# Kernel tuning notes

Hardware: AMD Instinct MI355X
Metric: run time of the kernel (lower is better)

The kernel has to match this reference:

```python
import jax, jax.numpy as jnp
import numpy as np

VOCAB, EMB = 30000, 300
HEADS, DPH = 8, 50
AD = HEADS * DPH            # att_dim_total = 400
MAX_LINES, MAX_WPL = 128, 32
BATCH = 16
NEG = 1e7                   # padding-mask penalty, matches torch source


def _split_heads(x):
    # [N, S, AD] -> [N, H, S, D]
    return x.reshape(x.shape[0], -1, HEADS, DPH).transpose(0, 2, 1, 3)


def _attention(q, k, v, mask_q=None, mask_k=None, mask_v=None):
    # Faithful port of MTHiSAN._attention. Note the (oddly named) torch masks:
    #   mask_q masks the KEY axis of scores, mask_k/mask_v zero the QUERY axis.
    scale = float(np.sqrt(q.shape[-1]))
    scores = jnp.einsum('bhqd,bhkd->bhqk', q, k) / scale
    if mask_q is not None:
        scores = scores - NEG * (~mask_q)[:, None, None, :].astype(scores.dtype)
    w = jax.nn.softmax(scores, axis=-1)
    if mask_k is not None:
        w = w * mask_k[:, None, :, None].astype(w.dtype)
    out = jnp.einsum('bhqk,bhkd->bhqd', w, v)
    if mask_v is not None:
        out = out * mask_v[:, None, :, None].astype(out.dtype)
    return out


def _forward(docs, emb, wq_w, wq_b, wk_w, wk_b, wv_w, wv_b, w_tgt,
             lq_w, lq_b, lk_w, lk_b, lv_w, lv_b, l_tgt,
             fc1_w, fc1_b, fc2_w, fc2_b):
    B = docs.shape[0]
    d = docs[:, :MAX_LINES * MAX_WPL].reshape(B * MAX_LINES, MAX_WPL)
    mask_w = d != 0                               # [B*L, W]
    mask_l = mask_w.sum(-1) != 0                  # [B*L]  non-empty lines
    # NOTE: instead of gathering non-empty lines (data-dependent shape), we keep
    # full shapes; masked word attention yields exact zeros for empty lines,
    # equivalent to the torch scatter into new_zeros.
    we = emb[d]                                   # [B*L, W, E] (dropout = eval/no-op)
    wq = jax.nn.elu(_split_heads(we @ wq_w + wq_b))
    wk = jax.nn.elu(_split_heads(we @ wk_w + wk_b))
    wv = jax.nn.elu(_split_heads(we @ wv_w + wv_b))
    watt = _attention(wq, wk, wv, mask_w, mask_w, mask_w)   # [B*L,H,W,D]
    # learned word-level target query (Linear(1, AD)(ones) == weight vector)
    tgt = jnp.broadcast_to(w_tgt.reshape(1, HEADS, 1, DPH),
                           (B * MAX_LINES, HEADS, 1, DPH))
    line_e = _attention(tgt, wk, watt, mask_q=mask_w)       # [B*L,H,1,D]
    line_e = line_e.transpose(0, 2, 1, 3).reshape(B * MAX_LINES, AD)
    line_e = line_e * mask_l[:, None].astype(line_e.dtype)  # zero empty lines
    line_e = line_e.reshape(B, MAX_LINES, AD)
    mask_l2 = mask_l.reshape(B, MAX_LINES)
    lq = jax.nn.elu(_split_heads(line_e @ lq_w + lq_b))
    lk = jax.nn.elu(_split_heads(line_e @ lk_w + lk_b))
    lv = jax.nn.elu(_split_heads(line_e @ lv_w + lv_b))
    latt = _attention(lq, lk, lv, mask_l2, mask_l2, mask_l2)  # [B,H,L,D]
    dtgt = jnp.broadcast_to(l_tgt.reshape(1, HEADS, 1, DPH), (B, HEADS, 1, DPH))
    doc_e = _attention(dtgt, lk, latt, mask_q=mask_l2)        # [B,H,1,D]
    doc_e = doc_e.transpose(0, 2, 1, 3).reshape(B, AD)
    logits1 = doc_e @ fc1_w + fc1_b   # task 'site'      [B,70]
    logits2 = doc_e @ fc2_w + fc2_b   # task 'histology' [B,512]
    return jnp.concatenate([logits1, logits2], axis=1)


def setup_inputs() -> dict:
    key = jax.random.key(0)
    ks = jax.random.split(key, 20)
    xavier = lambda k, i, o: (jax.random.normal(k, (i, o), jnp.float32)
                              * np.float32(np.sqrt(2.0 / (i + o))))
    emb = jax.random.normal(ks[0], (VOCAB, EMB), jnp.float32) * 0.02
    emb = emb.at[0].set(0.0)  # padding row zeroed as in __init__
    docs = jax.random.randint(ks[1], (BATCH, MAX_LINES * MAX_WPL), 0, VOCAB)
    z = lambda n: jnp.zeros((n,), jnp.float32)
    return dict(
        docs=docs, emb=emb,
        wq_w=xavier(ks[2], EMB, AD), wq_b=z(AD),
        wk_w=xavier(ks[3], EMB, AD), wk_b=z(AD),
        wv_w=xavier(ks[4], EMB, AD), wv_b=z(AD),
        w_tgt=jax.random.uniform(ks[5], (AD,), jnp.float32),
        lq_w=xavier(ks[6], AD, AD), lq_b=z(AD),
        lk_w=xavier(ks[7], AD, AD), lk_b=z(AD),
        lv_w=xavier(ks[8], AD, AD), lv_b=z(AD),
        l_tgt=jax.random.uniform(ks[9], (AD,), jnp.float32),
        fc1_w=xavier(ks[10], AD, 70), fc1_b=z(70),
        fc2_w=xavier(ks[11], AD, 512), fc2_b=z(512),
    )


def reference(docs, emb, wq_w, wq_b, wk_w, wk_b, wv_w, wv_b, w_tgt,
              lq_w, lq_b, lk_w, lk_b, lv_w, lv_b, l_tgt,
              fc1_w, fc1_b, fc2_w, fc2_b):
    return _forward(docs, emb, wq_w, wq_b, wk_w, wk_b, wv_w, wv_b, w_tgt,
                    lq_w, lq_b, lk_w, lk_b, lv_w, lv_b, l_tgt,
                    fc1_w, fc1_b, fc2_w, fc2_b)
```

## Files before the change

kernel.cpp:

```cpp
#include <hip/hip_runtime.h>
#include <math.h>

#define NLINES 2048
#define WPL 32
#define EMBD 300
#define AD 400
#define NH 8
#define DPH 50
#define QKV_S 52
#define SC_S 36
#define BATCH 16
#define LPD 128
#define NCOLS 1200
#define NPAD 1280
#define HBLK 4992
#define QP 54

typedef __bf16 bf16;
typedef bf16  v8bf  __attribute__((ext_vector_type(8)));
typedef float v16f  __attribute__((ext_vector_type(16)));

__device__ __forceinline__ float elu(float x) {
    return x > 0.f ? x : expm1f(x);
}
__device__ __forceinline__ float elu_fast(float x) {
    return x > 0.f ? x : (__expf(x) - 1.f);
}

__device__ __forceinline__ v8bf ntload8(const bf16* p) {
    return __builtin_nontemporal_load((const v8bf*)p);
}

#define SCALE 7.0710678118654755f

__global__ void split_rows_packed(const float* __restrict__ src,
                                  bf16* __restrict__ pk,
                                  int rows, int K, int K2)
{
    long idx = (long)blockIdx.x * 256 + threadIdx.x;
    if (idx >= (long)rows * K2) return;
    int r = (int)(idx / K2), k = (int)(idx - (long)r * K2);
    float x = (k < K) ? src[(long)r * K + k] : 0.f;
    bf16 h = (bf16)x;
    float hf = (float)h;
    bf16 l = (bf16)(x - hf);
    const long p = ((long)r * (K2 >> 3) + (k >> 3)) * 16 + (k & 7);
    pk[p] = h; pk[p + 8] = l;
}

__global__ void split_wt_packed(const float* __restrict__ W0, const float* __restrict__ W1,
                                const float* __restrict__ W2,
                                const float* __restrict__ B0, const float* __restrict__ B1,
                                const float* __restrict__ B2,
                                bf16* __restrict__ pk,
                                float* __restrict__ biasCat, int K, int K2)
{
    long idx = (long)blockIdx.x * 256 + threadIdx.x;
    if (idx >= (long)NPAD * K2) return;
    int n = (int)(idx / K2), k = (int)(idx - (long)n * K2);
    float x = 0.f;
    if (k < K && n < NCOLS) {
        int p = n / 400, c = n - p * 400;
        const float* W = (p == 0) ? W0 : (p == 1) ? W1 : W2;
        x = W[(long)k * 400 + c];
    }
    bf16 h = (bf16)x;
    float hf = (float)h;
    bf16 l = (bf16)(x - hf);
    const long pidx = ((long)(k >> 3) * NPAD + n) * 16 + (k & 7);
    pk[pidx] = h; pk[pidx + 8] = l;
    if (k == 0) {
        float b = 0.f;
        if (n < NCOLS) {
            int p = n / 400, c = n - p * 400;
            const float* Bp = (p == 0) ? B0 : (p == 1) ? B1 : B2;
            b = Bp[c];
        }
        biasCat[n] = b;
    }
}

__launch_bounds__(512, 2)
__global__ void fused_word(const bf16* __restrict__ Ap,
                           const int* __restrict__ docs,
                           const bf16* __restrict__ Bp,
                           const float* __restrict__ biasCat,
                           const float* __restrict__ w_tgt,
                           float* __restrict__ line_e, float* __restrict__ mask_l)
{
    __shared__ __align__(16) bf16 Alds[40 * 2 * 32 * 8];
    __shared__ __align__(16) float qkv[3][32][QP];
    __shared__ float sc[32 * 33];
    __shared__ float part[16][33];
    __shared__ float vpart[8][64];
    __shared__ float tw[WPL];
    __shared__ float coefA[WPL];
    __shared__ float cw[WPL];
    __shared__ float tg[52];
    __shared__ float msk[WPL];
    __shared__ float mls_s;

    const int tid = threadIdx.x;
    const int line = blockIdx.x;

    if (tid < WPL) msk[tid] = (docs[line * WPL + tid] != 0) ? 1.f : 0.f;
    __syncthreads();
    if (tid == 0) {
        float m = 0.f;
        for (int w = 0; w < WPL; ++w) m = fmaxf(m, msk[w]);
        mls_s = m;
        mask_l[line] = m;
    }

    for (int slot = tid; slot < 40 * 2 * 32; slot += 512) {
        const int row = slot & 31;
        const int hl  = (slot >> 5) & 1;
        const int kf  = slot >> 6;
        const int token = docs[line * WPL + row];
        *(v8bf*)&Alds[slot * 8] = ntload8(&Ap[((long)token * 40 + kf) * 16 + hl * 8]);
    }
    __syncthreads();

    const int wv = tid >> 6;
    const int lane = tid & 63;
    const int half = lane >> 5, r32 = lane & 31;

    for (int h = 0; h < NH; ++h) {
        if (wv < 6) {
            const int proj = wv >> 1;
            const int c0 = proj * 400 + h * 50 + (wv & 1) * 32;
            v16f a0 = (v16f)0.f, a1 = (v16f)0.f, a2 = (v16f)0.f;
            #pragma unroll 4
            for (int s = 0; s < 20; ++s) {
                const int kf = 2 * s + half;
                const v8bf fah = *(const v8bf*)&Alds[((kf * 2 + 0) * 32 + r32) * 8];
                const v8bf fal = *(const v8bf*)&Alds[((kf * 2 + 1) * 32 + r32) * 8];
                const bf16* bg = Bp + ((long)kf * NPAD + c0 + r32) * 16;
                const v8bf fbh = *(const v8bf*)&bg[0];
                const v8bf fbl = *(const v8bf*)&bg[8];
                a0 = __builtin_amdgcn_mfma_f32_32x32x16_bf16(fah, fbh, a0, 0, 0, 0);
                a1 = __builtin_amdgcn_mfma_f32_32x32x16_bf16(fah, fbl, a1, 0, 0, 0);
                a2 = __builtin_amdgcn_mfma_f32_32x32x16_bf16(fal, fbh, a2, 0, 0, 0);
            }
            const int d = (wv & 1) * 32 + r32;
            if (d < DPH) {
                const float bv = biasCat[c0 + r32];
                #pragma unroll
                for (int rg = 0; rg < 16; ++rg) {
                    const int row = (rg & 3) + 8 * (rg >> 2) + 4 * half;
                    qkv[proj][row][d] = elu_fast(a0[rg] + a1[rg] + a2[rg] + bv);
                }
            }
        } else {
            const int t = tid - 384;
            if (t < 96) {
                const int p = t / 32, row = t & 31;
                qkv[p][row][50] = 0.f; qkv[p][row][51] = 0.f;
                qkv[p][row][52] = 0.f; qkv[p][row][53] = 0.f;
            } else if (t >= 96 && t < 148) {
                const int i = t - 96;
                tg[i] = (i < DPH) ? w_tgt[h * DPH + i] : 0.f;
            }
        }
        __syncthreads();

        const float* q   = &qkv[0][0][0];
        const float* kk_ = &qkv[1][0][0];
        const float* vv_ = &qkv[2][0][0];

        const int j = tid >> 4, kg = tid & 15;
        float2 qv[27];
        #pragma unroll
        for (int i = 0; i < 27; ++i) qv[i] = *(const float2*)&q[j * QP + 2 * i];

        float e2[2];
        float m = -1e30f;
        #pragma unroll
        for (int c = 0; c < 2; ++c) {
            const int kk = kg * 2 + c;
            const float* kr = &kk_[kk * QP];
            float s = 0.f;
            #pragma unroll
            for (int i = 0; i < 27; ++i)
                s += qv[i].x * kr[2 * i] + qv[i].y * kr[2 * i + 1];
            s = s / SCALE - 1e7f * (1.f - msk[kk]);
            e2[c] = s;
            m = fmaxf(m, s);
        }
        m = fmaxf(m, __shfl_xor(m, 1, 16));
        m = fmaxf(m, __shfl_xor(m, 2, 16));
        m = fmaxf(m, __shfl_xor(m, 4, 16));
        m = fmaxf(m, __shfl_xor(m, 8, 16));
        float rsum = 0.f;
        #pragma unroll
        for (int c = 0; c < 2; ++c) { e2[c] = __expf(e2[c] - m); rsum += e2[c]; }
        rsum += __shfl_xor(rsum, 1, 16);
        rsum += __shfl_xor(rsum, 2, 16);
        rsum += __shfl_xor(rsum, 4, 16);
        rsum += __shfl_xor(rsum, 8, 16);
        sc[j * 33 + kg * 2]     = e2[0];
        sc[j * 33 + kg * 2 + 1] = e2[1];

        if (tid < WPL) {
            const float* kr = &kk_[tid * QP];
            float s = 0.f;
            #pragma unroll
            for (int i = 0; i < 25; ++i)
                s += tg[2 * i] * kr[2 * i] + tg[2 * i + 1] * kr[2 * i + 1];
            s = s / SCALE - 1e7f * (1.f - msk[tid]);
            float tm = s;
            #pragma unroll
            for (int off = 16; off >= 1; off >>= 1) tm = fmaxf(tm, __shfl_xor(tm, off, 32));
            const float te = __expf(s - tm);
            float tsum = te;
            #pragma unroll
            for (int off = 16; off >= 1; off >>= 1) tsum += __shfl_xor(tsum, off, 32);
            tw[tid] = te / tsum;
        }
        __syncthreads();

        if (kg == 0) coefA[j] = tw[j] * msk[j] / rsum;
        __syncthreads();

        {
            const int k = tid & 31, jg = tid >> 5;
            const int j0 = jg * 2;
            part[jg][k] = coefA[j0] * sc[j0 * 33 + k]
                        + coefA[j0 + 1] * sc[(j0 + 1) * 33 + k];
        }
        __syncthreads();
        if (tid < WPL) {
            float cv = 0.f;
            #pragma unroll
            for (int g = 0; g < 16; ++g) cv += part[g][tid];
            cw[tid] = cv;
        }
        __syncthreads();

        {
            const int d = tid & 63, kh = tid >> 6;
            float acc = 0.f;
            if (d < QP) {
                #pragma unroll
                for (int t = 0; t < 4; ++t) {
                    const int k = kh * 4 + t;
                    acc += cw[k] * vv_[k * QP + d];
                }
            }
            vpart[kh][d] = acc;
        }
        __syncthreads();
        if (tid < DPH) {
            float o = 0.f;
            #pragma unroll
            for (int g = 0; g < 8; ++g) o += vpart[g][tid];
            line_e[(long)line * AD + h * DPH + tid] = o * mls_s;
        }
        __syncthreads();
    }
}

__launch_bounds__(256, 4)
__global__ void mfma_gemm(const bf16* __restrict__ Ap,
                          const int* __restrict__ docs,
                          const bf16* __restrict__ Bp,
                          const float* __restrict__ biasCat,
                          float* __restrict__ C, int K2, int word_layout)
{
    __shared__ int tok[128];

    const int tid = threadIdx.x;

    const int total = (int)(gridDim.x * gridDim.y);
    int flat = (int)(blockIdx.y * gridDim.x + blockIdx.x);
    if ((total & 7) == 0) flat = (flat & 7) * (total >> 3) + (flat >> 3);
    const int bx = flat % (int)gridDim.x;
    const int by = flat / (int)gridDim.x;
    const int row0 = by * 128;
    const int n0 = bx * 128;

    if (tid < 128) tok[tid] = docs ? docs[row0 + tid] : (row0 + tid);
    __syncthreads();

    const int wv = tid >> 6, lane = tid & 63;
    const int half = lane >> 5, r32 = lane & 31;
    const int wm0 = (wv >> 1) * 64, wn0 = (wv & 1) * 64;

    const int colA = n0 + wn0 + r32;
    const int colB = colA + 32;

    const long a0 = (long)tok[wm0 + r32]      * ((long)K2 * 2);
    const long a1 = (long)tok[wm0 + 32 + r32] * ((long)K2 * 2);

    v16f acc[2][2];
    #pragma unroll
    for (int a = 0; a < 2; ++a)
        #pragma unroll
        for (int b = 0; b < 2; ++b) acc[a][b] = (v16f)0.f;

    const int nk = K2 >> 5;
    for (int kt = 0; kt < nk; ++kt) {
        #pragma unroll
        for (int ks = 0; ks < 2; ++ks) {
            const int k0 = kt * 32 + (ks * 2 + half) * 8;
            const bf16* bg = Bp + (long)(k0 >> 3) * NPAD * 16;
            const long ka = (long)k0 * 2;
            v8bf fb_h[2], fb_l[2], fa_h[2], fa_l[2];
            fb_h[0] = *(const v8bf*)&bg[(long)colA * 16];
            fb_l[0] = *(const v8bf*)&bg[(long)colA * 16 + 8];
            fb_h[1] = *(const v8bf*)&bg[(long)colB * 16];
            fb_l[1] = *(const v8bf*)&bg[(long)colB * 16 + 8];
            fa_h[0] = *(const v8bf*)&Ap[a0 + ka];
            fa_l[0] = *(const v8bf*)&Ap[a0 + ka + 8];
            fa_h[1] = *(const v8bf*)&Ap[a1 + ka];
            fa_l[1] = *(const v8bf*)&Ap[a1 + ka + 8];

            #pragma unroll
            for (int mt = 0; mt < 2; ++mt)
                #pragma unroll
                for (int nt = 0; nt < 2; ++nt)
                    acc[mt][nt] = __builtin_amdgcn_mfma_f32_32x32x16_bf16(fa_h[mt], fb_h[nt], acc[mt][nt], 0, 0, 0);
            #pragma unroll
            for (int mt = 0; mt < 2; ++mt)
                #pragma unroll
                for (int nt = 0; nt < 2; ++nt)
                    acc[mt][nt] = __builtin_amdgcn_mfma_f32_32x32x16_bf16(fa_h[mt], fb_l[nt], acc[mt][nt], 0, 0, 0);
            #pragma unroll
            for (int mt = 0; mt < 2; ++mt)
                #pragma unroll
                for (int nt = 0; nt < 2; ++nt)
                    acc[mt][nt] = __builtin_amdgcn_mfma_f32_32x32x16_bf16(fa_l[mt], fb_h[nt], acc[mt][nt], 0, 0, 0);
        }
    }

    if (word_layout) {
        #pragma unroll
        for (int nt = 0; nt < 2; ++nt) {
            const int col = n0 + wn0 + nt * 32 + r32;
            if (col >= NCOLS) continue;
            const float bv = biasCat[col];
            const int p = col / 400;
            const int rem = col - p * 400;
            const int hh = rem / 50;
            const int d  = rem - hh * 50;
            #pragma unroll
            for (int mt = 0; mt < 2; ++mt) {
                const int rbase = row0 + wm0 + mt * 32 + 4 * half;
                #pragma unroll
                for (int rg = 0; rg < 16; ++rg) {
                    const int row = rbase + (rg & 3) + 8 * (rg >> 2);
                    const int ln = row >> 5, r = row & 31;
                    const long base = (((long)ln * NH + hh) * 3 + p) * 1664 + r * 52;
                    const float x = acc[mt][nt][rg] + bv;
                    C[base + d] = elu_fast(x);
                    if (d == 49) {
                        float2 z; z.x = 0.f; z.y = 0.f;
                        *(float2*)&C[base + 50] = z;
                    }
                }
            }
        }
    } else {
        #pragma unroll
        for (int nt = 0; nt < 2; ++nt) {
            const int col = n0 + wn0 + nt * 32 + r32;
            if (col >= NCOLS) continue;
            const float bv = biasCat[col];
            #pragma unroll
            for (int mt = 0; mt < 2; ++mt) {
                const int rbase = row0 + wm0 + mt * 32 + 4 * half;
                #pragma unroll
                for (int rg = 0; rg < 16; ++rg) {
                    const int row = rbase + (rg & 3) + 8 * (rg >> 2);
                    const float x = acc[mt][nt][rg] + bv;
                    C[(long)row * NCOLS + col] = elu_fast(x);
                }
            }
        }
    }
}

__launch_bounds__(256)
__global__ void line_attn2(const float* __restrict__ Q, const float* __restrict__ Kp,
                           const float* __restrict__ Vp,
                           long DS, long HS, long LS,
                           const float* __restrict__ l_tgt, const float* __restrict__ mask_l,
                           float* __restrict__ doc_e)
{
    __shared__ float kl[LPD * 52];
    __shared__ float sc[64 * 130];
    __shared__ float ml[LPD];
    __shared__ float tw[LPD];
    __shared__ float cw[LPD];
    __shared__ float coefA[64];
    __shared__ float pm[4 * 64];
    __shared__ float ps[4 * 64];
    __shared__ float tg[52];
    __shared__ float rr[2];
    __shared__ float vpart[2][64];

    const int tid = threadIdx.x;
    const int doc = blockIdx.x >> 3;
    const int h = blockIdx.x & 7;
    const float* qbase = Q + doc * DS + h * HS;
    const float* kbase = Kp + doc * DS + h * HS;
    const float* vbase = Vp + doc * DS + h * HS;

    if (tid < LPD) { ml[tid] = mask_l[doc * LPD + tid]; cw[tid] = 0.f; }
    if (tid < 52) tg[tid] = (tid < DPH) ? l_tgt[h * DPH + tid] : 0.f;
    for (int idx = tid; idx < LPD * 52; idx += 256) {
        const int r = idx / 52, d = idx - r * 52;
        kl[idx] = (d < DPH) ? kbase[(long)r * LS + d] : 0.f;
    }
    __syncthreads();

    if (tid < LPD) {
        const float* kr = &kl[tid * 52];
        float s = 0.f;
        #pragma unroll
        for (int i = 0; i < 25; ++i)
            s += tg[2 * i] * kr[2 * i] + tg[2 * i + 1] * kr[2 * i + 1];
        tw[tid] = s / SCALE - 1e7f * (1.f - ml[tid]);
    }
    __syncthreads();
    if (tid < 64) {
        float a = fmaxf(tw[tid], tw[64 + tid]);
        #pragma unroll
        for (int off = 32; off >= 1; off >>= 1) a = fmaxf(a, __shfl_xor(a, off));
        if (tid == 0) rr[0] = a;
    }
    __syncthreads();
    if (tid < 64) {
        const float tm2 = rr[0];
        float a = __expf(tw[tid] - tm2) + __expf(tw[64 + tid] - tm2);
        #pragma unroll
        for (int off = 32; off >= 1; off >>= 1) a += __shfl_xor(a, off);
        if (tid == 0) rr[1] = a;
    }
    __syncthreads();
    if (tid < LPD) tw[tid] = __expf(tw[tid] - rr[0]) / rr[1];
    __syncthreads();

    const int j2 = tid & 63;
    const int kq = tid >> 6;

    for (int g = 0; g < 2; ++g) {
        const int j = g * 64 + j2;
        float2 qv[25];
        #pragma unroll
        for (int i = 0; i < 25; ++i)
            qv[i] = *(const float2*)(qbase + (long)j * LS + 2 * i);

        float m = -1e30f;
        for (int c = 0; c < 32; ++c) {
            const int k = kq * 32 + c;
            const float* kr = &kl[k * 52];
            float s = 0.f;
            #pragma unroll
            for (int i = 0; i < 25; ++i)
                s += qv[i].x * kr[2 * i] + qv[i].y * kr[2 * i + 1];
            s = s / SCALE - 1e7f * (1.f - ml[k]);
            sc[j2 * 130 + k] = s;
            m = fmaxf(m, s);
        }
        pm[kq * 64 + j2] = m;
        __syncthreads();
        const float rowm = fmaxf(fmaxf(pm[j2], pm[64 + j2]),
                                 fmaxf(pm[128 + j2], pm[192 + j2]));
        float sum = 0.f;
        for (int c = 0; c < 32; ++c) {
            const int k = kq * 32 + c;
            const float e = __expf(sc[j2 * 130 + k] - rowm);
            sc[j2 * 130 + k] = e;
            sum += e;
        }
        ps[kq * 64 + j2] = sum;
        __syncthreads();
        if (kq == 0) {
            const float rs = ps[j2] + ps[64 + j2] + ps[128 + j2] + ps[192 + j2];
            coefA[j2] = tw[j] * ml[j] / rs;
        }
        __syncthreads();
        if (tid < LPD) {
            float cv = 0.f;
            for (int jj = 0; jj < 64; ++jj)
                cv += coefA[jj] * sc[jj * 130 + tid];
            cw[tid] += cv;
        }
        __syncthreads();
    }

    const int d = tid & 63;
    const int half = (tid >> 6) & 1;
    if (tid < 128 && d < DPH) {
        float acc = 0.f;
        for (int k = half * 64; k < half * 64 + 64; ++k)
            acc += cw[k] * vbase[(long)k * LS + d];
        vpart[half][d] = acc;
    }
    __syncthreads();
    if (tid < DPH)
        doc_e[doc * AD + h * DPH + tid] = vpart[0][tid] + vpart[1][tid];
}

__launch_bounds__(256)
__global__ void word_attn(const float* __restrict__ qkv, const int* __restrict__ docs,
                          const float* __restrict__ w_tgt,
                          float* __restrict__ line_e, float* __restrict__ mask_l)
{
    __shared__ float qs[WPL * QKV_S];
    __shared__ float ks[WPL * QKV_S];
    __shared__ float vs[WPL * QKV_S];
    __shared__ float sc[WPL * SC_S];
    __shared__ float ts[WPL], tw[WPL], cw[WPL], msk[WPL];
    __shared__ float mls;

    const int tid = threadIdx.x;
    const int line = blockIdx.x;

    if (tid < WPL) msk[tid] = (docs[line * WPL + tid] != 0) ? 1.f : 0.f;
    __syncthreads();
    if (tid == 0) {
        float ml = 0.f;
        for (int w = 0; w < WPL; ++w) ml = fmaxf(ml, msk[w]);
        mls = ml;
        mask_l[line] = ml;
    }
    for (int h = 0; h < NH; ++h) {
        for (int idx = tid; idx < WPL * DPH; idx += 256) {
            const int r = idx / DPH, d = idx - r * DPH;
            const size_t base = (size_t)(line * WPL + r) * NCOLS + h * DPH + d;
            qs[r * QKV_S + d] = qkv[base];
            ks[r * QKV_S + d] = qkv[base + 400];
            vs[r * QKV_S + d] = qkv[base + 800];
        }
        __syncthreads();
        {
            const int j = tid >> 3, kg = tid & 7;
            #pragma unroll
            for (int c = 0; c < 4; ++c) {
                const int kk = kg * 4 + c;
                float s = 0.f;
                for (int dd = 0; dd < DPH; ++dd)
                    s += qs[j * QKV_S + dd] * ks[kk * QKV_S + dd];
                sc[j * SC_S + kk] = s / SCALE - 1e7f * (1.f - msk[kk]);
            }
        }
        if (tid < WPL) {
            float s = 0.f;
            for (int dd = 0; dd < DPH; ++dd)
                s += w_tgt[h * DPH + dd] * ks[tid * QKV_S + dd];
            ts[tid] = s / SCALE - 1e7f * (1.f - msk[tid]);
        }
        __syncthreads();
        if (tid < WPL) {
            const int j = tid;
            float m = -1e30f;
            for (int kk = 0; kk < WPL; ++kk) m = fmaxf(m, sc[j * SC_S + kk]);
            float sum = 0.f;
            for (int kk = 0; kk < WPL; ++kk) {
                const float e = expf(sc[j * SC_S + kk] - m);
                sc[j * SC_S + kk] = e;
                sum += e;
            }
            const float inv = 1.f / sum;
            for (int kk = 0; kk < WPL; ++kk) sc[j * SC_S + kk] *= inv;
        } else if (tid == WPL) {
            float m = -1e30f;
            for (int jj = 0; jj < WPL; ++jj) m = fmaxf(m, ts[jj]);
            float sum = 0.f;
            for (int jj = 0; jj < WPL; ++jj) { const float e = expf(ts[jj] - m); tw[jj] = e; sum += e; }
            const float inv = 1.f / sum;
            for (int jj = 0; jj < WPL; ++jj) tw[jj] *= inv;
        }
        __syncthreads();
        if (tid < WPL) {
            const int kk = tid;
            float c = 0.f;
            for (int jj = 0; jj < WPL; ++jj) c += tw[jj] * msk[jj] * sc[jj * SC_S + kk];
            cw[kk] = c;
        }
        __syncthreads();
        if (tid < DPH) {
            float acc = 0.f;
            for (int kk = 0; kk < WPL; ++kk) acc += cw[kk] * vs[kk * QKV_S + tid];
            line_e[line * AD + h * DPH + tid] = acc * mls;
        }
        __syncthreads();
    }
}

__launch_bounds__(256, 2)
__global__ void gemm_qkv(const float* __restrict__ Asrc,
                         const int* __restrict__ docs,
                         const float* __restrict__ emb,
                         const float* __restrict__ W0, const float* __restrict__ W1,
                         const float* __restrict__ W2,
                         const float* __restrict__ B0, const float* __restrict__ B1,
                         const float* __restrict__ B2,
                         float* __restrict__ C, int M, int K)
{
    __shared__ __align__(16) float As[32][132];
    __shared__ __align__(16) float Bs[32][132];

    const int tid = threadIdx.x;
    const int row0 = blockIdx.x * 128;
    const int n0 = blockIdx.y * 128;
    const int tc = tid & 15, tr = tid >> 4;

    float acc[2][2][4][4];
    #pragma unroll
    for (int a = 0; a < 2; ++a)
        #pragma unroll
        for (int b = 0; b < 2; ++b)
            #pragma unroll
            for (int c = 0; c < 4; ++c)
                #pragma unroll
                for (int d = 0; d < 4; ++d) acc[a][b][c][d] = 0.f;

    const int ma = tid & 127;
    const int kq = tid >> 7;
    const float* arow;
    if (docs) arow = emb + (size_t)docs[row0 + ma] * EMBD;
    else      arow = Asrc + (size_t)(row0 + ma) * K;

    const int gcol = n0 + ma;
    const int p = gcol / 400;
    const int ccol = gcol - p * 400;
    const float* Wp = (p == 0) ? W0 : (p == 1) ? W1 : W2;
    const bool colv = gcol < NCOLS;

    const int nk = (K + 31) >> 5;
    for (int ck = 0; ck < nk; ++ck) {
        const int k0 = ck * 32;
        #pragma unroll
        for (int f = 0; f < 4; ++f) {
            const int kl = kq * 16 + f * 4;
            const int kg = k0 + kl;
            float4 v = make_float4(0.f, 0.f, 0.f, 0.f);
            if (kg < K) v = *(const float4*)(arow + kg);
            As[kl + 0][ma] = v.x;
            As[kl + 1][ma] = v.y;
            As[kl + 2][ma] = v.z;
            As[kl + 3][ma] = v.w;
        }
        #pragma unroll
        for (int i = 0; i < 16; ++i) {
            const int kl = kq * 16 + i;
            const int kg = k0 + kl;
            float v = 0.f;
            if (colv && kg < K) v = Wp[(size_t)kg * 400 + ccol];
            Bs[kl][ma] = v;
        }
        __syncthreads();

        #pragma unroll 8
        for (int k = 0; k < 32; ++k) {
            const float4 a0 = *(const float4*)&As[k][tr * 4];
            const float4 a1 = *(const float4*)&As[k][64 + tr * 4];
            const float4 b0 = *(const float4*)&Bs[k][tc * 4];
            const float4 b1 = *(const float4*)&Bs[k][64 + tc * 4];
            const float ar[2][4] = {{a0.x, a0.y, a0.z, a0.w}, {a1.x, a1.y, a1.z, a1.w}};
            const float br[2][4] = {{b0.x, b0.y, b0.z, b0.w}, {b1.x, b1.y, b1.z, b1.w}};
            #pragma unroll
            for (int im = 0; im < 2; ++im)
                #pragma unroll
                for (int in_ = 0; in_ < 2; ++in_)
                    #pragma unroll
                    for (int rr = 0; rr < 4; ++rr)
                        #pragma unroll
                        for (int cc = 0; cc < 4; ++cc)
                            acc[im][in_][rr][cc] += ar[im][rr] * br[in_][cc];
        }
        __syncthreads();
    }

    #pragma unroll
    for (int in_ = 0; in_ < 2; ++in_) {
        const int ncol = n0 + in_ * 64 + tc * 4;
        if (ncol >= NCOLS) continue;
        const int pj = ncol / 400;
        const int cj = ncol - pj * 400;
        const float* Bp = (pj == 0) ? B0 : (pj == 1) ? B1 : B2;
        const float4 bv = *(const float4*)(Bp + cj);
        #pragma unroll
        for (int im = 0; im < 2; ++im) {
            #pragma unroll
            for (int rr = 0; rr < 4; ++rr) {
                const int row = row0 + im * 64 + tr * 4 + rr;
                float4 o;
                o.x = elu(acc[im][in_][rr][0] + bv.x);
                o.y = elu(acc[im][in_][rr][1] + bv.y);
                o.z = elu(acc[im][in_][rr][2] + bv.z);
                o.w = elu(acc[im][in_][rr][3] + bv.w);
                *(float4*)(C + (size_t)row * NCOLS + ncol) = o;
            }
        }
    }
}

__global__ void logits_kernel(const float* __restrict__ doc_e,
                              const float* __restrict__ fc1_w, const float* __restrict__ fc1_b,
                              const float* __restrict__ fc2_w, const float* __restrict__ fc2_b,
                              float* __restrict__ out)
{
    int o = blockIdx.x * blockDim.x + threadIdx.x;
    if (o >= BATCH * 582) return;
    int b = o / 582, jj = o - b * 582;
    const float* de = doc_e + b * AD;
    float acc;
    if (jj < 70) {
        acc = fc1_b[jj];
        for (int k = 0; k < AD; ++k) acc += de[k] * fc1_w[k * 70 + jj];
    } else {
        int j2 = jj - 70;
        acc = fc2_b[j2];
        for (int k = 0; k < AD; ++k) acc += de[k] * fc2_w[k * 512 + j2];
    }
    out[o] = acc;
}

extern "C" void kernel_launch(void* const* d_in, const int* in_sizes, int n_in,
                              void* d_out, int out_size, void* d_ws, size_t ws_size,
                              hipStream_t stream) {
    const int*   docs  = (const int*)  d_in[0];
    const float* emb   = (const float*)d_in[1];
    const float* wq_w  = (const float*)d_in[2];
    const float* wq_b  = (const float*)d_in[3];
    const float* wk_w  = (const float*)d_in[4];
    const float* wk_b  = (const float*)d_in[5];
    const float* wv_w  = (const float*)d_in[6];
    const float* wv_b  = (const float*)d_in[7];
    const float* w_tgt = (const float*)d_in[8];
    const float* lq_w  = (const float*)d_in[9];
    const float* lq_b  = (const float*)d_in[10];
    const float* lk_w  = (const float*)d_in[11];
    const float* lk_b  = (const float*)d_in[12];
    const float* lv_w  = (const float*)d_in[13];
    const float* lv_b  = (const float*)d_in[14];
    const float* l_tgt = (const float*)d_in[15];
    const float* fc1_w = (const float*)d_in[16];
    const float* fc1_b = (const float*)d_in[17];
    const float* fc2_w = (const float*)d_in[18];
    const float* fc2_b = (const float*)d_in[19];
    float* out = (float*)d_out;
    float* ws = (float*)d_ws;

    const long O_LINE_E = 0;
    const long O_MASK_L = 819200;
    const long O_DOC_E  = 821248;
    const long O_BIAS_W = 827648;
    const long O_BIAS_L = 828928;
    const long O_EMB_H  = 830208;
    const long O_WTW_H  = 10430208;
    const long O_WTL_H  = 10839808;
    const long O_LE_H   = 11372288;
    const long O_R      = 12224256;

    const long LINE_QKV_FL = (long)NLINES * NCOLS;
    long ws_fl = (long)(ws_size / 4);
    long Rcap = ws_fl - O_R;

    if (Rcap >= LINE_QKV_FL) {
        float* line_e = ws + O_LINE_E;
        float* mask_l = ws + O_MASK_L;
        float* doc_e  = ws + O_DOC_E;
        float* bias_w = ws + O_BIAS_W;
        float* bias_l = ws + O_BIAS_L;
        bf16* embp = (bf16*)(ws + O_EMB_H);
        bf16* wtwp = (bf16*)(ws + O_WTW_H);
        bf16* wtlp = (bf16*)(ws + O_WTL_H);
        bf16* lep  = (bf16*)(ws + O_LE_H);
        float* R   = ws + O_R;

        split_rows_packed<<<(30000L * 320 + 255) / 256, 256, 0, stream>>>(emb, embp, 30000, 300, 320);
        split_wt_packed<<<((long)NPAD * 320 + 255) / 256, 256, 0, stream>>>(wq_w, wk_w, wv_w,
                                                                            wq_b, wk_b, wv_b,
                                                                            wtwp, bias_w, 300, 320);
        split_wt_packed<<<((long)NPAD * 416 + 255) / 256, 256, 0, stream>>>(lq_w, lk_w, lv_w,
                                                                            lq_b, lk_b, lv_b,
                                                                            wtlp, bias_l, 400, 416);

        fused_word<<<NLINES, 512, 0, stream>>>(embp, docs, wtwp, bias_w, w_tgt,
                                               line_e, mask_l);

        split_rows_packed<<<((long)NLINES * 416 + 255) / 256, 256, 0, stream>>>(line_e, lep,
                                                                                NLINES, 400, 416);
        dim3 g2(10, NLINES / 128);
        mfma_gemm<<<g2, 256, 0, stream>>>(lep, nullptr, wtlp, bias_l, R, 416, 0);
        line_attn2<<<BATCH * NH, 256, 0, stream>>>(R, R + 400, R + 800,
                                                   (long)LPD * NCOLS, (long)DPH, (long)NCOLS,
                                                   l_tgt, mask_l, doc_e);
        logits_kernel<<<(BATCH * 582 + 255) / 256, 256, 0, stream>>>(doc_e, fc1_w, fc1_b,
                                                                     fc2_w, fc2_b, out);
    } else {
        const long F_FIXED = 827648;
        const long PER_LINE_FL = (long)WPL * NCOLS;
        float* line_e = ws;
        float* mask_l = ws + 819200;
        float* doc_e  = ws + 821248;
        float* R      = ws + F_FIXED;
        long Rcap2 = ws_fl - F_FIXED;

        long maxl = Rcap2 / PER_LINE_FL;
        if (maxl > NLINES) maxl = NLINES;
        long maxl4 = (maxl / 4) * 4;
        int nc = (int)((NLINES + maxl4 - 1) / maxl4);
        int chunk = (int)((NLINES + nc - 1) / nc);
        chunk = ((chunk + 3) / 4) * 4;

        for (int c0 = 0; c0 < NLINES; c0 += chunk) {
            int cl = NLINES - c0 < chunk ? NLINES - c0 : chunk;
            dim3 g1((cl * 32) / 128, 10);
            gemm_qkv<<<g1, 256, 0, stream>>>(nullptr, docs + (size_t)c0 * WPL, emb,
                                             wq_w, wk_w, wv_w, wq_b, wk_b, wv_b,
                                             R, cl * 32, EMBD);
            word_attn<<<cl, 256, 0, stream>>>(R, docs + (size_t)c0 * WPL, w_tgt,
                                              line_e + (size_t)c0 * AD, mask_l + c0);
        }
        dim3 g2(16, 10);
        gemm_qkv<<<g2, 256, 0, stream>>>(line_e, nullptr, emb,
                                         lq_w, lk_w, lv_w, lq_b, lk_b, lv_b,
                                         R, NLINES, AD);
        line_attn2<<<BATCH * NH, 256, 0, stream>>>(R, R + 400, R + 800,
                                                   (long)LPD * NCOLS, (long)DPH, (long)NCOLS,
                                                   l_tgt, mask_l, doc_e);
        logits_kernel<<<(BATCH * 582 + 255) / 256, 256, 0, stream>>>(doc_e, fc1_w, fc1_b,
                                                                     fc2_w, fc2_b, out);
    }
}
```

Before: 574.6 us.

## Restructure word attention epilogue to cut barriers using 32-lane shuffle reductions

Rewrites the per-head attention tail of fused_word so each 32-lane group computes scores for two query rows plus the target row against its key, then does the softmax reductions with shuffles instead of going through shared memory. The final weighted sum over V is also done with shuffle reductions. Together these remove several shared arrays and about four __syncthreads per head. The cost is more redundant key loads and extra shuffle traffic per thread, since each thread now computes three dot products.

New measurement: 604.7 us. +5.2%, slower.

```diff
diff --git a/kernel.cpp b/kernel.cpp
--- a/kernel.cpp
+++ b/kernel.cpp
@@ -90,13 +90,8 @@
 {
     __shared__ __align__(16) bf16 Alds[40 * 2 * 32 * 8];
     __shared__ __align__(16) float qkv[3][32][QP];
-    __shared__ float sc[32 * 33];
     __shared__ float part[16][33];
-    __shared__ float vpart[8][64];
-    __shared__ float tw[WPL];
-    __shared__ float coefA[WPL];
-    __shared__ float cw[WPL];
-    __shared__ float tg[52];
+    __shared__ float tg[56];
     __shared__ float msk[WPL];
     __shared__ float mls_s;
 
@@ -157,104 +152,76 @@
                 const int p = t / 32, row = t & 31;
                 qkv[p][row][50] = 0.f; qkv[p][row][51] = 0.f;
                 qkv[p][row][52] = 0.f; qkv[p][row][53] = 0.f;
-            } else if (t >= 96 && t < 148) {
+            } else if (t >= 96 && t < 152) {
                 const int i = t - 96;
                 tg[i] = (i < DPH) ? w_tgt[h * DPH + i] : 0.f;
             }
         }
         __syncthreads();
 
-        const float* q   = &qkv[0][0][0];
-        const float* kk_ = &qkv[1][0][0];
-        const float* vv_ = &qkv[2][0][0];
-
-        const int j = tid >> 4, kg = tid & 15;
-        float2 qv[27];
-        #pragma unroll
-        for (int i = 0; i < 27; ++i) qv[i] = *(const float2*)&q[j * QP + 2 * i];
-
-        float e2[2];
-        float m = -1e30f;
-        #pragma unroll
-        for (int c = 0; c < 2; ++c) {
-            const int kk = kg * 2 + c;
-            const float* kr = &kk_[kk * QP];
-            float s = 0.f;
-            #pragma unroll
-            for (int i = 0; i < 27; ++i)
-                s += qv[i].x * kr[2 * i] + qv[i].y * kr[2 * i + 1];
-            s = s / SCALE - 1e7f * (1.f - msk[kk]);
-            e2[c] = s;
-            m = fmaxf(m, s);
-        }
-        m = fmaxf(m, __shfl_xor(m, 1, 16));
-        m = fmaxf(m, __shfl_xor(m, 2, 16));
-        m = fmaxf(m, __shfl_xor(m, 4, 16));
-        m = fmaxf(m, __shfl_xor(m, 8, 16));
-        float rsum = 0.f;
-        #pragma unroll
-        for (int c = 0; c < 2; ++c) { e2[c] = __expf(e2[c] - m); rsum += e2[c]; }
-        rsum += __shfl_xor(rsum, 1, 16);
-        rsum += __shfl_xor(rsum, 2, 16);
-        rsum += __shfl_xor(rsum, 4, 16);
-        rsum += __shfl_xor(rsum, 8, 16);
-        sc[j * 33 + kg * 2]     = e2[0];
-        sc[j * 33 + kg * 2 + 1] = e2[1];
-
-        if (tid < WPL) {
-            const float* kr = &kk_[tid * QP];
-            float s = 0.f;
-            #pragma unroll
-            for (int i = 0; i < 25; ++i)
-                s += tg[2 * i] * kr[2 * i] + tg[2 * i + 1] * kr[2 * i + 1];
-            s = s / SCALE - 1e7f * (1.f - msk[tid]);
-            float tm = s;
-            #pragma unroll
-            for (int off = 16; off >= 1; off >>= 1) tm = fmaxf(tm, __shfl_xor(tm, off, 32));
-            const float te = __expf(s - tm);
-            float tsum = te;
-            #pragma unroll
-            for (int off = 16; off >= 1; off >>= 1) tsum += __shfl_xor(tsum, off, 32);
-            tw[tid] = te / tsum;
-        }
-        __syncthreads();
-
-        if (kg == 0) coefA[j] = tw[j] * msk[j] / rsum;
-        __syncthreads();
-
         {
-            const int k = tid & 31, jg = tid >> 5;
-            const int j0 = jg * 2;
-            part[jg][k] = coefA[j0] * sc[j0 * 33 + k]
-                        + coefA[j0 + 1] * sc[(j0 + 1) * 33 + k];
-        }
-        __syncthreads();
-        if (tid < WPL) {
-            float cv = 0.f;
-            #pragma unroll
-            for (int g = 0; g < 16; ++g) cv += part[g][tid];
-            cw[tid] = cv;
+            const int slot = tid >> 5;
+            const int k = tid & 31;
+            const int j0 = slot * 2, j1 = j0 + 1;
+            const float* Krow = &qkv[1][k][0];
+            const float* Q0   = &qkv[0][j0][0];
+            const float* Q1   = &qkv[0][j1][0];
+            float s0 = 0.f, s1 = 0.f, st = 0.f;
+            #pragma unroll
+            for (int i = 0; i < 27; ++i) {
+                const float2 kv = *(const float2*)&Krow[2 * i];
+                const float2 q0 = *(const float2*)&Q0[2 * i];
+                const float2 q1 = *(const float2*)&Q1[2 * i];
+                const float2 tv = *(const float2*)&tg[2 * i];
+                s0 += q0.x * kv.x + q0.y * kv.y;
+                s1 += q1.x * kv.x + q1.y * kv.y;
+                st += tv.x * kv.x + tv.y * kv.y;
+            }
+            const float pen = 1e7f * (1.f - msk[k]);
+            s0 = s0 / SCALE - pen;
+            s1 = s1 / SCALE - pen;
+            st = st / SCALE - pen;
+
+            float m0 = s0, m1 = s1, mt = st;
+            #pragma unroll
+            for (int off = 16; off >= 1; off >>= 1) {
+                m0 = fmaxf(m0, __shfl_xor(m0, off, 32));
+                m1 = fmaxf(m1, __shfl_xor(m1, off, 32));
+                mt = fmaxf(mt, __shfl_xor(mt, off, 32));
+            }
+            const float e0 = __expf(s0 - m0);
+            const float e1 = __expf(s1 - m1);
+            const float et = __expf(st - mt);
+            float r0 = e0, r1 = e1, rt = et;
+            #pragma unroll
+            for (int off = 16; off >= 1; off >>= 1) {
+                r0 += __shfl_xor(r0, off, 32);
+                r1 += __shfl_xor(r1, off, 32);
+                rt += __shfl_xor(rt, off, 32);
+            }
+            const float tw_k = et / rt;
+            const float c0 = __shfl(tw_k, j0, 32) * msk[j0] / r0;
+            const float c1 = __shfl(tw_k, j1, 32) * msk[j1] / r1;
+            part[slot][k] = c0 * e0 + c1 * e1;
         }
         __syncthreads();
 
         {
-            const int d = tid & 63, kh = tid >> 6;
-            float acc = 0.f;
-            if (d < QP) {
-                #pragma unroll
-                for (int t = 0; t < 4; ++t) {
-                    const int k = kh * 4 + t;
-                    acc += cw[k] * vv_[k * QP + d];
-                }
-            }
-            vpart[kh][d] = acc;
-        }
-        __syncthreads();
-        if (tid < DPH) {
-            float o = 0.f;
-            #pragma unroll
-            for (int g = 0; g < 8; ++g) o += vpart[g][tid];
-            line_e[(long)line * AD + h * DPH + tid] = o * mls_s;
+            const int slot = tid >> 5;
+            const int k = tid & 31;
+            float cwk = 0.f;
+            #pragma unroll
+            for (int g = 0; g < 16; ++g) cwk += part[g][k];
+            #pragma unroll
+            for (int di = 0; di < 4; ++di) {
+                const int d = slot * 4 + di;
+                float p = (d < DPH) ? cwk * qkv[2][k][d] : 0.f;
+                #pragma unroll
+                for (int off = 16; off >= 1; off >>= 1)
+                    p += __shfl_xor(p, off, 32);
+                if (k == 0 && d < DPH)
+                    line_e[(long)line * AD + h * DPH + d] = p * mls_s;
+            }
         }
         __syncthreads();
     }
```

## Process two lines per fused_word block to reuse weight fragments across lines

Applied to the files above, without the earlier changes.

Each fused_word block now handles two document lines. Every B-weight fragment loaded from global memory feeds MFMAs for both lines, so weight traffic per line is halved. The attention phase splits the 512 threads into two 256-thread halves, one per line, with each thread covering more keys. The price is double the LDS footprint, more accumulator registers, launch bounds lowered to one block per CU, and half as many blocks, which may reduce occupancy and latency hiding.

Result: slower. 632.0 us (+10.0%).

```diff
diff --git a/kernel.cpp b/kernel.cpp
--- a/kernel.cpp
+++ b/kernel.cpp
@@ -80,7 +80,7 @@
     }
 }
 
-__launch_bounds__(512, 2)
+__launch_bounds__(512, 1)
 __global__ void fused_word(const bf16* __restrict__ Ap,
                            const int* __restrict__ docs,
                            const bf16* __restrict__ Bp,
@@ -88,36 +88,44 @@
                            const float* __restrict__ w_tgt,
                            float* __restrict__ line_e, float* __restrict__ mask_l)
 {
-    __shared__ __align__(16) bf16 Alds[40 * 2 * 32 * 8];
-    __shared__ __align__(16) float qkv[3][32][QP];
-    __shared__ float sc[32 * 33];
-    __shared__ float part[16][33];
-    __shared__ float vpart[8][64];
-    __shared__ float tw[WPL];
-    __shared__ float coefA[WPL];
-    __shared__ float cw[WPL];
-    __shared__ float tg[52];
-    __shared__ float msk[WPL];
-    __shared__ float mls_s;
+    __shared__ __align__(16) bf16 Alds[2][40 * 2 * 32 * 8];
+    __shared__ __align__(16) float qkv[2][3][32][QP];
+    __shared__ float sc[2][32 * 33];
+    __shared__ float part[2][8][33];
+    __shared__ float vpart[2][4][64];
+    __shared__ float tw[2][WPL];
+    __shared__ float coefA[2][WPL];
+    __shared__ float cw[2][WPL];
+    __shared__ float tg[56];
+    __shared__ float msk[2][WPL];
+    __shared__ float mls_s[2];
 
     const int tid = threadIdx.x;
-    const int line = blockIdx.x;
-
-    if (tid < WPL) msk[tid] = (docs[line * WPL + tid] != 0) ? 1.f : 0.f;
-    __syncthreads();
-    if (tid == 0) {
+    const int line0 = blockIdx.x * 2;
+
+    if (tid < 2 * WPL) {
+        const int li = tid >> 5, w = tid & 31;
+        msk[li][w] = (docs[(line0 + li) * WPL + w] != 0) ? 1.f : 0.f;
+    }
+    __syncthreads();
+    if (tid < 2) {
         float m = 0.f;
-        for (int w = 0; w < WPL; ++w) m = fmaxf(m, msk[w]);
-        mls_s = m;
-        mask_l[line] = m;
-    }
-
-    for (int slot = tid; slot < 40 * 2 * 32; slot += 512) {
-        const int row = slot & 31;
-        const int hl  = (slot >> 5) & 1;
-        const int kf  = slot >> 6;
-        const int token = docs[line * WPL + row];
-        *(v8bf*)&Alds[slot * 8] = ntload8(&Ap[((long)token * 40 + kf) * 16 + hl * 8]);
+        for (int w = 0; w < WPL; ++w) m = fmaxf(m, msk[tid][w]);
+        mls_s[tid] = m;
+        mask_l[line0 + tid] = m;
+    }
+
+    for (int g = tid; g < 2 * 2560; g += 512) {
+        const int li = g >> 11;
+        const int slot = g & 2047;
+        const int li2 = g / 2560;
+        const int s2  = g - li2 * 2560;
+        const int row = s2 & 31;
+        const int hl  = (s2 >> 5) & 1;
+        const int kf  = s2 >> 6;
+        const int token = docs[(line0 + li2) * WPL + row];
+        (void)li; (void)slot;
+        *(v8bf*)&Alds[li2][s2 * 8] = ntload8(&Ap[((long)token * 40 + kf) * 16 + hl * 8]);
     }
     __syncthreads();
 
@@ -129,18 +137,26 @@
         if (wv < 6) {
             const int proj = wv >> 1;
             const int c0 = proj * 400 + h * 50 + (wv & 1) * 32;
-            v16f a0 = (v16f)0.f, a1 = (v16f)0.f, a2 = (v16f)0.f;
+            v16f p0 = (v16f)0.f, p1 = (v16f)0.f, p2 = (v16f)0.f;
+            v16f q0 = (v16f)0.f, q1 = (v16f)0.f, q2 = (v16f)0.f;
             #pragma unroll 4
             for (int s = 0; s < 20; ++s) {
                 const int kf = 2 * s + half;
-                const v8bf fah = *(const v8bf*)&Alds[((kf * 2 + 0) * 32 + r32) * 8];
-                const v8bf fal = *(const v8bf*)&Alds[((kf * 2 + 1) * 32 + r32) * 8];
                 const bf16* bg = Bp + ((long)kf * NPAD + c0 + r32) * 16;
                 const v8bf fbh = *(const v8bf*)&bg[0];
                 const v8bf fbl = *(const v8bf*)&bg[8];
-                a0 = __builtin_amdgcn_mfma_f32_32x32x16_bf16(fah, fbh, a0, 0, 0, 0);
-                a1 = __builtin_amdgcn_mfma_f32_32x32x16_bf16(fah, fbl, a1, 0, 0, 0);
-                a2 = __builtin_amdgcn_mfma_f32_32x32x16_bf16(fal, fbh, a2, 0, 0, 0);
+                const int ea = ((kf * 2 + 0) * 32 + r32) * 8;
+                const int eb = ((kf * 2 + 1) * 32 + r32) * 8;
+                const v8bf fah0 = *(const v8bf*)&Alds[0][ea];
+                const v8bf fal0 = *(const v8bf*)&Alds[0][eb];
+                const v8bf fah1 = *(const v8bf*)&Alds[1][ea];
+                const v8bf fal1 = *(const v8bf*)&Alds[1][eb];
+                p0 = __builtin_amdgcn_mfma_f32_32x32x16_bf16(fah0, fbh, p0, 0, 0, 0);
+                q0 = __builtin_amdgcn_mfma_f32_32x32x16_bf16(fah1, fbh, q0, 0, 0, 0);
+                p1 = __builtin_amdgcn_mfma_f32_32x32x16_bf16(fah0, fbl, p1, 0, 0, 0);
+                q1 = __builtin_amdgcn_mfma_f32_32x32x16_bf16(fah1, fbl, q1, 0, 0, 0);
+                p2 = __builtin_amdgcn_mfma_f32_32x32x16_bf16(fal0, fbh, p2, 0, 0, 0);
+                q2 = __builtin_amdgcn_mfma_f32_32x32x16_bf16(fal1, fbh, q2, 0, 0, 0);
             }
             const int d = (wv & 1) * 32 + r32;
             if (d < DPH) {
@@ -148,66 +164,68 @@
                 #pragma unroll
                 for (int rg = 0; rg < 16; ++rg) {
                     const int row = (rg & 3) + 8 * (rg >> 2) + 4 * half;
-                    qkv[proj][row][d] = elu_fast(a0[rg] + a1[rg] + a2[rg] + bv);
+                    qkv[0][proj][row][d] = elu_fast(p0[rg] + p1[rg] + p2[rg] + bv);
+                    qkv[1][proj][row][d] = elu_fast(q0[rg] + q1[rg] + q2[rg] + bv);
                 }
             }
         } else {
             const int t = tid - 384;
-            if (t < 96) {
-                const int p = t / 32, row = t & 31;
-                qkv[p][row][50] = 0.f; qkv[p][row][51] = 0.f;
-                qkv[p][row][52] = 0.f; qkv[p][row][53] = 0.f;
-            } else if (t >= 96 && t < 148) {
-                const int i = t - 96;
-                tg[i] = (i < DPH) ? w_tgt[h * DPH + i] : 0.f;
-            }
-        }
-        __syncthreads();
-
-        const float* q   = &qkv[0][0][0];
-        const float* kk_ = &qkv[1][0][0];
-        const float* vv_ = &qkv[2][0][0];
-
-        const int j = tid >> 4, kg = tid & 15;
+            for (int idx = t; idx < 192; idx += 128) {
+                const int li = idx / 96;
+                const int rem = idx - li * 96;
+                const int p = rem / 32, row = rem & 31;
+                qkv[li][p][row][50] = 0.f; qkv[li][p][row][51] = 0.f;
+                qkv[li][p][row][52] = 0.f; qkv[li][p][row][53] = 0.f;
+            }
+            if (t < 56) tg[t] = (t < DPH) ? w_tgt[h * DPH + t] : 0.f;
+        }
+        __syncthreads();
+
+        const int li = tid >> 8;
+        const int t  = tid & 255;
+        const float* q   = &qkv[li][0][0][0];
+        const float* kk_ = &qkv[li][1][0][0];
+        const float* vv_ = &qkv[li][2][0][0];
+        const float* mk  = &msk[li][0];
+
+        const int j = t >> 3, kg = t & 7;
         float2 qv[27];
         #pragma unroll
         for (int i = 0; i < 27; ++i) qv[i] = *(const float2*)&q[j * QP + 2 * i];
 
-        float e2[2];
+        float e4[4];
         float m = -1e30f;
         #pragma unroll
-        for (int c = 0; c < 2; ++c) {
-            const int kk = kg * 2 + c;
+        for (int c = 0; c < 4; ++c) {
+            const int kk = kg * 4 + c;
             const float* kr = &kk_[kk * QP];
             float s = 0.f;
             #pragma unroll
             for (int i = 0; i < 27; ++i)
                 s += qv[i].x * kr[2 * i] + qv[i].y * kr[2 * i + 1];
-            s = s / SCALE - 1e7f * (1.f - msk[kk]);
-            e2[c] = s;
+            s = s / SCALE - 1e7f * (1.f - mk[kk]);
+            e4[c] = s;
             m = fmaxf(m, s);
         }
-        m = fmaxf(m, __shfl_xor(m, 1, 16));
-        m = fmaxf(m, __shfl_xor(m, 2, 16));
-        m = fmaxf(m, __shfl_xor(m, 4, 16));
-        m = fmaxf(m, __shfl_xor(m, 8, 16));
+        m = fmaxf(m, __shfl_xor(m, 1));
+        m = fmaxf(m, __shfl_xor(m, 2));
+        m = fmaxf(m, __shfl_xor(m, 4));
         float rsum = 0.f;
         #pragma unroll
-        for (int c = 0; c < 2; ++c) { e2[c] = __expf(e2[c] - m); rsum += e2[c]; }
-        rsum += __shfl_xor(rsum, 1, 16);
-        rsum += __shfl_xor(rsum, 2, 16);
-        rsum += __shfl_xor(rsum, 4, 16);
-        rsum += __shfl_xor(rsum, 8, 16);
-        sc[j * 33 + kg * 2]     = e2[0];
-        sc[j * 33 + kg * 2 + 1] = e2[1];
-
-        if (tid < WPL) {
-            const float* kr = &kk_[tid * QP];
+        for (int c = 0; c < 4; ++c) { e4[c] = __expf(e4[c] - m); rsum += e4[c]; }
+        rsum += __shfl_xor(rsum, 1);
+        rsum += __shfl_xor(rsum, 2);
+        rsum += __shfl_xor(rsum, 4);
+        #pragma unroll
+        for (int c = 0; c < 4; ++c) sc[li][j * 33 + kg * 4 + c] = e4[c];
+
+        if (t < WPL) {
+            const float* kr = &kk_[t * QP];
             float s = 0.f;
             #pragma unroll
             for (int i = 0; i < 25; ++i)
                 s += tg[2 * i] * kr[2 * i] + tg[2 * i + 1] * kr[2 * i + 1];
-            s = s / SCALE - 1e7f * (1.f - msk[tid]);
+            s = s / SCALE - 1e7f * (1.f - mk[t]);
             float tm = s;
             #pragma unroll
             for (int off = 16; off >= 1; off >>= 1) tm = fmaxf(tm, __shfl_xor(tm, off, 32));
@@ -215,46 +233,49 @@
             float tsum = te;
             #pragma unroll
             for (int off = 16; off >= 1; off >>= 1) tsum += __shfl_xor(tsum, off, 32);
-            tw[tid] = te / tsum;
-        }
-        __syncthreads();
-
-        if (kg == 0) coefA[j] = tw[j] * msk[j] / rsum;
+            tw[li][t] = te / tsum;
+        }
+        __syncthreads();
+
+        if (kg == 0) coefA[li][j] = tw[li][j] * mk[j] / rsum;
         __syncthreads();
 
         {
-            const int k = tid & 31, jg = tid >> 5;
-            const int j0 = jg * 2;
-            part[jg][k] = coefA[j0] * sc[j0 * 33 + k]
-                        + coefA[j0 + 1] * sc[(j0 + 1) * 33 + k];
-        }
-        __syncthreads();
-        if (tid < WPL) {
+            const int k = t & 31, jg = t >> 5;
             float cv = 0.f;
             #pragma unroll
-            for (int g = 0; g < 16; ++g) cv += part[g][tid];
-            cw[tid] = cv;
+            for (int u = 0; u < 4; ++u) {
+                const int jj = jg * 4 + u;
+                cv += coefA[li][jj] * sc[li][jj * 33 + k];
+            }
+            part[li][jg][k] = cv;
+        }
+        __syncthreads();
+        if (t < WPL) {
+            float cv = 0.f;
+            #pragma unroll
+            for (int g = 0; g < 8; ++g) cv += part[li][g][t];
+            cw[li][t] = cv;
         }
         __syncthreads();
 
         {
-            const int d = tid & 63, kh = tid >> 6;
+            const int d = t & 63, kh = t >> 6;
             float acc = 0.f;
             if (d < QP) {
                 #pragma unroll
-                for (int t = 0; t < 4; ++t) {
-                    const int k = kh * 4 + t;
-                    acc += cw[k] * vv_[k * QP + d];
+                for (int u = 0; u < 8; ++u) {
+                    const int k = kh * 8 + u;
+                    acc += cw[li][k] * vv_[k * QP + d];
                 }
             }
-            vpart[kh][d] = acc;
-        }
-        __syncthreads();
-        if (tid < DPH) {
-            float o = 0.f;
-            #pragma unroll
-            for (int g = 0; g < 8; ++g) o += vpart[g][tid];
-            line_e[(long)line * AD + h * DPH + tid] = o * mls_s;
+            vpart[li][kh][d] = acc;
+        }
+        __syncthreads();
+        if (t < DPH) {
+            const float o = vpart[li][0][t] + vpart[li][1][t]
+                          + vpart[li][2][t] + vpart[li][3][t];
+            line_e[(long)(line0 + li) * AD + h * DPH + t] = o * mls_s[li];
         }
         __syncthreads();
     }
@@ -781,8 +802,8 @@
                                                                             lq_b, lk_b, lv_b,
                                                                             wtlp, bias_l, 400, 416);
 
-        fused_word<<<NLINES, 512, 0, stream>>>(embp, docs, wtwp, bias_w, w_tgt,
-                                               line_e, mask_l);
+        fused_word<<<NLINES / 2, 512, 0, stream>>>(embp, docs, wtwp, bias_w, w_tgt,
+                                                   line_e, mask_l);
 
         split_rows_packed<<<((long)NLINES * 416 + 255) / 256, 256, 0, stream>>>(line_e, lep,
                                                                                 NLINES, 400, 416);
```
